# Optimization experiments

Measured on AMD Instinct MI355X. Metric: run time of the kernel, lower is better.

Reference implementation:

```python
import jax, jax.numpy as jnp
import numpy as np


def setup_inputs() -> dict:
    key = jax.random.key(0)
    k_x, k_w = jax.random.split(key)
    x = jax.random.normal(k_x, (4096, 4096), dtype=jnp.float32)
    weight = jax.random.uniform(k_w, (7, 7), dtype=jnp.float32)
    bias = jnp.zeros((1,), dtype=jnp.float32)
    return {"x": x, "weight": weight, "bias": bias}


def reference(x, weight, bias):
    # Valid 2D cross-correlation (no kernel flip), matching corr2d, plus scalar bias.
    # lax.conv_general_dilated performs cross-correlation by default.
    lhs = x[None, None, :, :]            # [1, 1, H, W]
    rhs = weight[None, None, :, :]       # [1, 1, kh, kw]
    y = jax.lax.conv_general_dilated(
        lhs, rhs,
        window_strides=(1, 1),
        padding="VALID",
        dimension_numbers=("NCHW", "OIHW", "NCHW"),
    )[0, 0]                              # [H-kh+1, W-kw+1]
    return y + bias[0]
```

## Files before the change

### kernel.cpp

```cpp
#include <hip/hip_runtime.h>

#define WI 4096
#define HI 4096
#define WO 4090
#define HO 4090
#define TH 16
#define IH 22
#define LW 536
#define CPR4 134
#define NCHK (IH*CPR4)

typedef __attribute__((ext_vector_type(8))) short bf16x8;
typedef __attribute__((ext_vector_type(4))) float f32x4;

__device__ __forceinline__ unsigned short f2bf(float f) {
    union { float f; unsigned u; } v; v.f = f;
    unsigned r = v.u + 0x7FFFu + ((v.u >> 16) & 1u);
    return (unsigned short)(r >> 16);
}

__global__ __launch_bounds__(256, 4) void conv7x7(
    const float* __restrict__ x, const float* __restrict__ wgt,
    const float* __restrict__ bias, float* __restrict__ out)
{
    __shared__ unsigned short tile[IH * LW];
    __shared__ float wlds[49];

    const int tid = threadIdx.x;
    const int x0  = blockIdx.x * 512;
    const int y0  = blockIdx.y * TH;

    if (tid < 49) wlds[tid] = wgt[tid];
    const float bb = bias[0];

    #pragma unroll
    for (int k = 0; k < 12; ++k) {
        const int c = tid + (k << 8);
        if (c < NCHK) {
            const int row = c / CPR4;
            const int c4  = c - row * CPR4;
            int gy  = y0 + row;       gy  = gy  < HI ? gy : HI - 1;
            int gxs = x0 + (c4 << 2); gxs = gxs <= WI - 4 ? gxs : WI - 4;
            const float4 q = *(const float4*)(x + (size_t)gy * WI + gxs);
            unsigned u0 = (unsigned)f2bf(q.x) | ((unsigned)f2bf(q.y) << 16);
            unsigned u1 = (unsigned)f2bf(q.z) | ((unsigned)f2bf(q.w) << 16);
            *(uint2*)&tile[row * LW + (c4 << 2)] = make_uint2(u0, u1);
        }
    }
    __syncthreads();

    const int n   = tid & 15;
    const int kb8 = ((tid >> 4) & 3) << 3;
    bf16x8 Bf[7];
    #pragma unroll
    for (int ky = 0; ky < 7; ++ky) {
        #pragma unroll
        for (int j = 0; j < 8; ++j) {
            const int t = kb8 + j - n;
            const float wv = (t >= 0 && t < 7) ? wlds[ky * 7 + t] : 0.f;
            Bf[ky][j] = (short)f2bf(wv);
        }
    }

    const int wcol  = (tid >> 6) << 7;
    const int growb = y0 + (((tid >> 4) & 3) << 2);

    #pragma unroll
    for (int tp = 0; tp < 4; ++tp) {
        const int xt0 = wcol + (tp << 5);
        const int xt1 = xt0 + 16;
        f32x4 acc0 = {0.f, 0.f, 0.f, 0.f};
        f32x4 acc1 = {0.f, 0.f, 0.f, 0.f};
        #pragma unroll
        for (int ky = 0; ky < 7; ++ky) {
            const unsigned short* rp = &tile[(ky + n) * LW + kb8];
            const bf16x8 av0 = *(const bf16x8*)(rp + xt0);
            const bf16x8 av1 = *(const bf16x8*)(rp + xt1);
            acc0 = __builtin_amdgcn_mfma_f32_16x16x32_bf16(av0, Bf[ky], acc0, 0, 0, 0);
            acc1 = __builtin_amdgcn_mfma_f32_16x16x32_bf16(av1, Bf[ky], acc1, 0, 0, 0);
        }
        const int gc0 = x0 + xt0 + n;
        const int gc1 = gc0 + 16;
        #pragma unroll
        for (int v = 0; v < 4; ++v) {
            const int grow = growb + v;
            if (grow < HO) {
                if (gc0 < WO) out[(size_t)grow * WO + gc0] = acc0[v] + bb;
                if (gc1 < WO) out[(size_t)grow * WO + gc1] = acc1[v] + bb;
            }
        }
    }
}

extern "C" void kernel_launch(void* const* d_in, const int* in_sizes, int n_in,
                              void* d_out, int out_size, void* d_ws, size_t ws_size,
                              hipStream_t stream) {
    const float* x = (const float*)d_in[0];
    const float* w = (const float*)d_in[1];
    const float* b = (const float*)d_in[2];
    float* out = (float*)d_out;
    dim3 grid(8, 256);
    conv7x7<<<grid, 256, 0, stream>>>(x, w, b, out);
}
```

Before: 34.34 us.

## Pipeline row strips per block with async global-to-LDS loads and ring buffer

Each block now handles 64 output rows instead of 16, walking four 16-row strips. A 22-row bf16 ring buffer keeps the 6-row halo between strips, so input rows are no longer re-fetched by neighbouring blocks. The next strip's fp32 rows are issued with global_load_lds into an fp32 staging buffer while MFMA compute runs on the current strip, then converted to bf16. The cost is a large LDS footprint (about 71 KB), occupancy lowered to 2 blocks per CU, a quarter as many blocks, and extra barriers per strip.

```diff
diff --git a/kernel.cpp b/kernel.cpp
--- a/kernel.cpp
+++ b/kernel.cpp
@@ -4,11 +4,11 @@
 #define HI 4096
 #define WO 4090
 #define HO 4090
-#define TH 16
-#define IH 22
 #define LW 536
 #define CPR4 134
-#define NCHK (IH*CPR4)
+#define TROWS 22
+#define PCHK (22*CPR4)
+#define SCHK (16*CPR4)
 
 typedef __attribute__((ext_vector_type(8))) short bf16x8;
 typedef __attribute__((ext_vector_type(4))) float f32x4;
@@ -19,35 +19,23 @@
     return (unsigned short)(r >> 16);
 }
 
-__global__ __launch_bounds__(256, 4) void conv7x7(
+__device__ __forceinline__ void gl_lds16(const float* g, float* l) {
+    __builtin_amdgcn_global_load_lds(
+        (const __attribute__((address_space(1))) void*)g,
+        (__attribute__((address_space(3))) void*)l, 16, 0, 0);
+}
+
+__global__ __launch_bounds__(256, 2) void conv7x7(
     const float* __restrict__ x, const float* __restrict__ wgt,
     const float* __restrict__ bias, float* __restrict__ out)
 {
-    __shared__ unsigned short tile[IH * LW];
-    __shared__ float wlds[49];
+    __shared__ unsigned short bt[TROWS * LW];
+    __shared__ float fb[PCHK * 4];
 
     const int tid = threadIdx.x;
     const int x0  = blockIdx.x * 512;
-    const int y0  = blockIdx.y * TH;
-
-    if (tid < 49) wlds[tid] = wgt[tid];
+    const int yb  = blockIdx.y * 64;
     const float bb = bias[0];
-
-    #pragma unroll
-    for (int k = 0; k < 12; ++k) {
-        const int c = tid + (k << 8);
-        if (c < NCHK) {
-            const int row = c / CPR4;
-            const int c4  = c - row * CPR4;
-            int gy  = y0 + row;       gy  = gy  < HI ? gy : HI - 1;
-            int gxs = x0 + (c4 << 2); gxs = gxs <= WI - 4 ? gxs : WI - 4;
-            const float4 q = *(const float4*)(x + (size_t)gy * WI + gxs);
-            unsigned u0 = (unsigned)f2bf(q.x) | ((unsigned)f2bf(q.y) << 16);
-            unsigned u1 = (unsigned)f2bf(q.z) | ((unsigned)f2bf(q.w) << 16);
-            *(uint2*)&tile[row * LW + (c4 << 2)] = make_uint2(u0, u1);
-        }
-    }
-    __syncthreads();
 
     const int n   = tid & 15;
     const int kb8 = ((tid >> 4) & 3) << 3;
@@ -57,39 +45,93 @@
         #pragma unroll
         for (int j = 0; j < 8; ++j) {
             const int t = kb8 + j - n;
-            const float wv = (t >= 0 && t < 7) ? wlds[ky * 7 + t] : 0.f;
+            const float wv = (t >= 0 && t < 7) ? wgt[ky * 7 + t] : 0.f;
             Bf[ky][j] = (short)f2bf(wv);
         }
     }
 
-    const int wcol  = (tid >> 6) << 7;
-    const int growb = y0 + (((tid >> 4) & 3) << 2);
-
-    #pragma unroll
-    for (int tp = 0; tp < 4; ++tp) {
-        const int xt0 = wcol + (tp << 5);
-        const int xt1 = xt0 + 16;
-        f32x4 acc0 = {0.f, 0.f, 0.f, 0.f};
-        f32x4 acc1 = {0.f, 0.f, 0.f, 0.f};
+    auto stage_issue = [&](int rowbase, int nchk, int iters) {
+        for (int k = 0; k < iters; ++k) {
+            const int c = tid + (k << 8);
+            if (c < nchk) {
+                const int r  = c / CPR4;
+                const int c4 = c - r * CPR4;
+                int gy  = rowbase + r;    gy  = gy  < HI ? gy : HI - 1;
+                int gxs = x0 + (c4 << 2); gxs = gxs <= WI - 4 ? gxs : WI - 4;
+                gl_lds16(x + (size_t)gy * WI + gxs, fb + c * 4);
+            }
+        }
+    };
+    auto cvt = [&](int B, int nchk, int iters) {
+        for (int k = 0; k < iters; ++k) {
+            const int c = tid + (k << 8);
+            if (c < nchk) {
+                const int r  = c / CPR4;
+                const int c4 = c - r * CPR4;
+                int pr = B + r; if (pr >= TROWS) pr -= TROWS;
+                const float4 q = *(const float4*)(fb + c * 4);
+                unsigned u0 = (unsigned)f2bf(q.x) | ((unsigned)f2bf(q.y) << 16);
+                unsigned u1 = (unsigned)f2bf(q.z) | ((unsigned)f2bf(q.w) << 16);
+                *(uint2*)&bt[pr * LW + (c4 << 2)] = make_uint2(u0, u1);
+            }
+        }
+    };
+    auto compute = [&](int tb, int y0) {
+        int pr[7];
         #pragma unroll
         for (int ky = 0; ky < 7; ++ky) {
-            const unsigned short* rp = &tile[(ky + n) * LW + kb8];
-            const bf16x8 av0 = *(const bf16x8*)(rp + xt0);
-            const bf16x8 av1 = *(const bf16x8*)(rp + xt1);
-            acc0 = __builtin_amdgcn_mfma_f32_16x16x32_bf16(av0, Bf[ky], acc0, 0, 0, 0);
-            acc1 = __builtin_amdgcn_mfma_f32_16x16x32_bf16(av1, Bf[ky], acc1, 0, 0, 0);
+            int p = tb + ky + n; if (p >= TROWS) p -= TROWS; pr[ky] = p;
         }
-        const int gc0 = x0 + xt0 + n;
-        const int gc1 = gc0 + 16;
+        const int wcol  = (tid >> 6) << 7;
+        const int growb = y0 + (((tid >> 4) & 3) << 2);
         #pragma unroll
-        for (int v = 0; v < 4; ++v) {
-            const int grow = growb + v;
-            if (grow < HO) {
-                if (gc0 < WO) out[(size_t)grow * WO + gc0] = acc0[v] + bb;
-                if (gc1 < WO) out[(size_t)grow * WO + gc1] = acc1[v] + bb;
+        for (int tp = 0; tp < 4; ++tp) {
+            const int xt0 = wcol + (tp << 5);
+            const int xt1 = xt0 + 16;
+            f32x4 acc0 = {0.f, 0.f, 0.f, 0.f};
+            f32x4 acc1 = {0.f, 0.f, 0.f, 0.f};
+            #pragma unroll
+            for (int ky = 0; ky < 7; ++ky) {
+                const unsigned short* rp = &bt[pr[ky] * LW + kb8];
+                const bf16x8 av0 = *(const bf16x8*)(rp + xt0);
+                const bf16x8 av1 = *(const bf16x8*)(rp + xt1);
+                acc0 = __builtin_amdgcn_mfma_f32_16x16x32_bf16(av0, Bf[ky], acc0, 0, 0, 0);
+                acc1 = __builtin_amdgcn_mfma_f32_16x16x32_bf16(av1, Bf[ky], acc1, 0, 0, 0);
+            }
+            const int gc0 = x0 + xt0 + n;
+            const int gc1 = gc0 + 16;
+            #pragma unroll
+            for (int v = 0; v < 4; ++v) {
+                const int grow = growb + v;
+                if (grow < HO) {
+                    if (gc0 < WO) out[(size_t)grow * WO + gc0] = acc0[v] + bb;
+                    if (gc1 < WO) out[(size_t)grow * WO + gc1] = acc1[v] + bb;
+                }
             }
         }
-    }
+    };
+
+    stage_issue(yb, PCHK, 12);
+    __syncthreads();
+    cvt(0, PCHK, 12);
+    __syncthreads();
+
+    stage_issue(yb + 22, SCHK, 9);
+    compute(0, yb);
+    __syncthreads();
+    cvt(0, SCHK, 9);
+    __syncthreads();
+    stage_issue(yb + 38, SCHK, 9);
+    compute(16, yb + 16);
+    __syncthreads();
+    cvt(16, SCHK, 9);
+    __syncthreads();
+    stage_issue(yb + 54, SCHK, 9);
+    compute(10, yb + 32);
+    __syncthreads();
+    cvt(10, SCHK, 9);
+    __syncthreads();
+    compute(4, yb + 48);
 }
 
 extern "C" void kernel_launch(void* const* d_in, const int* in_sizes, int n_in,
@@ -99,6 +141,6 @@
     const float* w = (const float*)d_in[1];
     const float* b = (const float*)d_in[2];
     float* out = (float*)d_out;
-    dim3 grid(8, 256);
+    dim3 grid(8, 64);
     conv7x7<<<grid, 256, 0, stream>>>(x, w, b, out);
 }
```

After: 33.53 us. 1.02x faster.
